# Kernel optimization log

Measured on AMD Instinct MI355X. Metric: run time of the kernel, lower is better.

## Reference

```python
import jax, jax.numpy as jnp
import numpy as np

N = 50000
E = 800000
N_CT = 32
EMBED = 256
HIDDEN = 128
OUT = 512
NEG_SLOPE = 0.2


def setup_inputs() -> dict:
    key = jax.random.key(0)
    ks = jax.random.split(key, 12)
    ct_idx = jax.random.randint(ks[0], (N,), 0, N_CT)
    cell_type_onehot = jax.nn.one_hot(ct_idx, N_CT, dtype=jnp.float32)
    lipid_droplet_scalar = jax.random.normal(ks[1], (N,), dtype=jnp.float32)
    edge_index = jax.random.randint(ks[2], (2, E), 0, N, dtype=jnp.int32)
    s = 0.05
    return {
        "cell_type_onehot": cell_type_onehot,
        "lipid_droplet_scalar": lipid_droplet_scalar,
        "edge_index": edge_index,
        "W_embed": jax.random.normal(ks[3], (N_CT + 1, EMBED), dtype=jnp.float32) * s,
        "b_embed": jnp.zeros((EMBED,), dtype=jnp.float32),
        "W_l": jax.random.normal(ks[4], (EMBED, HIDDEN), dtype=jnp.float32) * s,
        "b_l": jnp.zeros((HIDDEN,), dtype=jnp.float32),
        "W_r": jax.random.normal(ks[5], (EMBED, HIDDEN), dtype=jnp.float32) * s,
        "b_r": jnp.zeros((HIDDEN,), dtype=jnp.float32),
        "att": jax.random.normal(ks[6], (HIDDEN,), dtype=jnp.float32) * s,
        "gat_bias": jnp.zeros((HIDDEN,), dtype=jnp.float32),
        "W_out": jax.random.normal(ks[7], (HIDDEN, OUT), dtype=jnp.float32) * s,
        "b_out": jnp.zeros((OUT,), dtype=jnp.float32),
        "dispersion": jax.random.normal(ks[8], (OUT, N_CT), dtype=jnp.float32) * s,
    }


def reference(cell_type_onehot, lipid_droplet_scalar, edge_index,
              W_embed, b_embed, W_l, b_l, W_r, b_r, att, gat_bias,
              W_out, b_out, dispersion):
    n = cell_type_onehot.shape[0]
    lds = lipid_droplet_scalar[:, None] if lipid_droplet_scalar.ndim == 1 else lipid_droplet_scalar
    combined = jnp.concatenate([cell_type_onehot, lds], axis=1)  # [N, n_ct+1]
    x = jax.nn.elu(combined @ W_embed + b_embed)  # [N, EMBED]

    # GATv2Conv, heads=1, concat=True (PyG semantics)
    x_l = x @ W_l + b_l  # source-side transform [N, H]
    x_r = x @ W_r + b_r  # target-side transform [N, H]
    src, dst = edge_index[0], edge_index[1]
    e = jax.nn.leaky_relu(x_l[src] + x_r[dst], negative_slope=NEG_SLOPE)  # [E, H]
    logit = e @ att  # [E]
    # scatter-softmax over incoming edges of each target node
    m = jax.ops.segment_max(logit, dst, num_segments=n)
    alpha = jnp.exp(logit - m[dst])
    denom = jax.ops.segment_sum(alpha, dst, num_segments=n)
    alpha = alpha / (denom[dst] + 1e-16)
    agg = jax.ops.segment_sum(alpha[:, None] * x_l[src], dst, num_segments=n)  # [N, H]
    h = jax.nn.elu(agg + gat_bias)

    logits = h @ W_out + b_out  # [N, OUT]
    ct_idx = jnp.argmax(cell_type_onehot, axis=1)  # [N]
    disp = jax.nn.softplus(dispersion[:, ct_idx]).T  # [N, OUT]
    return logits, disp
```

## Files before the change

kernel.cpp:

```cpp
#include <hip/hip_runtime.h>
#include <hip/hip_bf16.h>
#include <math.h>

#define N    50000
#define E    800000
#define NCT  32
#define EMB  256
#define HID  128
#define OUTD 512
#define NB_SCAN 49
#define XPAD 260
#define HPAD 132

__device__ __forceinline__ float4 fma4s(float a, float4 b, float4 c) {
    return make_float4(fmaf(a, b.x, c.x), fmaf(a, b.y, c.y),
                       fmaf(a, b.z, c.z), fmaf(a, b.w, c.w));
}
__device__ __forceinline__ float4 add4(float4 a, float4 b) {
    return make_float4(a.x + b.x, a.y + b.y, a.z + b.z, a.w + b.w);
}

__global__ void k_init(const float* __restrict__ onehot,
                       const float* __restrict__ dispersion,
                       int* __restrict__ ct, int* __restrict__ hist,
                       float* __restrict__ spt) {
    int i = blockIdx.x * 256 + threadIdx.x;
    if (i < N) {
        const float* row = onehot + (size_t)i * NCT;
        int c = 0;
        #pragma unroll
        for (int j = 0; j < NCT; j++)
            if (row[j] > 0.5f) c = j;
        ct[i] = c;
        hist[i] = 0;
    }
    if (i < OUTD * NCT) {
        float x = dispersion[i];
        float s = log1pf(expf(-fabsf(x))) + fmaxf(x, 0.f);
        int c = i >> 5, j = i & 31;
        spt[j * OUTD + c] = s;
    }
}

__global__ __launch_bounds__(256) void k_hist(const int* __restrict__ eidx,
                                              int* __restrict__ hist) {
    int i = blockIdx.x * 256 + threadIdx.x;
    if (i < E / 4) {
        int4 d = reinterpret_cast<const int4*>(eidx + E)[i];
        atomicAdd(&hist[d.x], 1);
        atomicAdd(&hist[d.y], 1);
        atomicAdd(&hist[d.z], 1);
        atomicAdd(&hist[d.w], 1);
    }
}

__global__ __launch_bounds__(256, 3) void k_xlr(
        const int* __restrict__ ct, const float* __restrict__ ldsc,
        const float* __restrict__ We, const float* __restrict__ be,
        const float* __restrict__ pWl, const float* __restrict__ pbl,
        const float* __restrict__ pWr, const float* __restrict__ pbr,
        float* __restrict__ xl, float* __restrict__ xr) {
    __shared__ float xs[32 * XPAD];
    __shared__ float Bs[16 * 256];
    __shared__ int   ctl[32];
    __shared__ float ldl[32];
    const int t  = threadIdx.x;
    const int n0 = blockIdx.x * 32;

    if (t < 32) {
        int n = n0 + t; if (n >= N) n = N - 1;
        ctl[t] = ct[n];
        ldl[t] = ldsc[n];
    }
    __syncthreads();

    {
        const float w32 = We[NCT * EMB + t];
        const float bb  = be[t];
        for (int m = 0; m < 32; m++) {
            float v = fmaf(ldl[m], w32, We[ctl[m] * EMB + t]) + bb;
            xs[m * XPAD + t] = v > 0.f ? v : expm1f(v);
        }
    }

    const int cg = t & 31;
    const int rg = t >> 5;
    const float* xrow = xs + rg * 4 * XPAD;
    const int cA = cg * 4;
    const int st_kk  = t >> 6;
    const int st_col = (t & 63) * 4;

    float4 accA[4], accB[4];
    #pragma unroll
    for (int r = 0; r < 4; r++) {
        accA[r] = make_float4(0.f, 0.f, 0.f, 0.f);
        accB[r] = make_float4(0.f, 0.f, 0.f, 0.f);
    }

    for (int kc = 0; kc < EMB; kc += 16) {
        __syncthreads();
        #pragma unroll
        for (int j = 0; j < 4; j++) {
            int kk  = st_kk + j * 4;
            int col = st_col;
            const float* src = (col < HID) ? (pWl + (size_t)(kc + kk) * HID + col)
                                           : (pWr + (size_t)(kc + kk) * HID + col - HID);
            *reinterpret_cast<float4*>(&Bs[kk * 256 + col]) =
                *reinterpret_cast<const float4*>(src);
        }
        __syncthreads();

        #pragma unroll
        for (int kk = 0; kk < 16; kk += 4) {
            float4 bA[4], bB[4];
            #pragma unroll
            for (int q = 0; q < 4; q++) {
                bA[q] = *reinterpret_cast<const float4*>(&Bs[(kk + q) * 256 + cA]);
                bB[q] = *reinterpret_cast<const float4*>(&Bs[(kk + q) * 256 + 128 + cA]);
            }
            float4 a[4];
            #pragma unroll
            for (int r = 0; r < 4; r++)
                a[r] = *reinterpret_cast<const float4*>(xrow + r * XPAD + kc + kk);
            #pragma unroll
            for (int r = 0; r < 4; r++) {
                accA[r] = fma4s(a[r].x, bA[0], accA[r]);
                accB[r] = fma4s(a[r].x, bB[0], accB[r]);
                accA[r] = fma4s(a[r].y, bA[1], accA[r]);
                accB[r] = fma4s(a[r].y, bB[1], accB[r]);
                accA[r] = fma4s(a[r].z, bA[2], accA[r]);
                accB[r] = fma4s(a[r].z, bB[2], accB[r]);
                accA[r] = fma4s(a[r].w, bA[3], accA[r]);
                accB[r] = fma4s(a[r].w, bB[3], accB[r]);
            }
        }
    }

    const float4 biasA = *reinterpret_cast<const float4*>(pbl + cA);
    const float4 biasB = *reinterpret_cast<const float4*>(pbr + cA);
    #pragma unroll
    for (int r = 0; r < 4; r++) {
        int n = n0 + rg * 4 + r;
        if (n < N) {
            *reinterpret_cast<float4*>(xl + (size_t)n * HID + cA) = add4(accA[r], biasA);
            *reinterpret_cast<float4*>(xr + (size_t)n * HID + cA) = add4(accB[r], biasB);
        }
    }
}

__global__ __launch_bounds__(1024) void k_scan1(const int* __restrict__ hist,
                                                int* __restrict__ offs,
                                                int* __restrict__ bsum) {
    __shared__ int sb[2][1024];
    const int t = threadIdx.x;
    const int i = blockIdx.x * 1024 + t;
    int v = (i < N) ? hist[i] : 0;
    sb[0][t] = v;
    __syncthreads();
    int pin = 0;
    for (int off = 1; off < 1024; off <<= 1) {
        int x = sb[pin][t];
        if (t >= off) x += sb[pin][t - off];
        sb[pin ^ 1][t] = x;
        pin ^= 1;
        __syncthreads();
    }
    int incl = sb[pin][t];
    if (i < N) offs[i] = incl - v;
    if (t == 1023) bsum[blockIdx.x] = incl;
}

__global__ void k_scan2(const int* __restrict__ bsum, int* __restrict__ bbase) {
    if (threadIdx.x == 0) {
        int run = 0;
        for (int j = 0; j < NB_SCAN; j++) { bbase[j] = run; run += bsum[j]; }
    }
}

__global__ __launch_bounds__(1024) void k_scan3(int* __restrict__ offs,
                                                int* __restrict__ cursor,
                                                const int* __restrict__ bbase) {
    const int t = threadIdx.x;
    const int i = blockIdx.x * 1024 + t;
    if (i < N) {
        int v = offs[i] + bbase[blockIdx.x];
        offs[i] = v;
        cursor[i] = v;
    }
    if (blockIdx.x == 0 && t == 0) offs[N] = E;
}

__global__ __launch_bounds__(256) void k_scatter(const int* __restrict__ eidx,
                                                 int* __restrict__ cursor,
                                                 int* __restrict__ sorted) {
    const int e = blockIdx.x * 256 + threadIdx.x;
    if (e < E) {
        int s = eidx[e];
        int d = eidx[E + e];
        int pos = atomicAdd(&cursor[d], 1);
        sorted[pos] = s;
    }
}

__global__ __launch_bounds__(256, 8) void k_agg(
        const int* __restrict__ offs, const int* __restrict__ srt,
        const float* __restrict__ xl, const float* __restrict__ attv,
        const float* __restrict__ gb, float* xrh) {
    const int t = threadIdx.x;
    const int n = blockIdx.x * 8 + (t >> 5);
    if (n >= N) return;
    const int lane = t & 31;
    const float4* xl4 = reinterpret_cast<const float4*>(xl);
    float4* xh4 = reinterpret_cast<float4*>(xrh);

    const float4 xr4 = xh4[(size_t)n * 32 + lane];
    const float4 at4 = reinterpret_cast<const float4*>(attv)[lane];
    const int i0  = offs[n];
    const int deg = offs[n + 1] - i0;

    float m = -3.0e38f, den = 0.f;
    float4 acc = make_float4(0.f, 0.f, 0.f, 0.f);

#define STEP(XC) {                                                          \
    float vx = XC.x + xr4.x, vy = XC.y + xr4.y,                             \
          vz = XC.z + xr4.z, vw = XC.w + xr4.w;                             \
    vx = fmaxf(vx, 0.f) + 0.2f * fminf(vx, 0.f);                            \
    vy = fmaxf(vy, 0.f) + 0.2f * fminf(vy, 0.f);                            \
    vz = fmaxf(vz, 0.f) + 0.2f * fminf(vz, 0.f);                            \
    vw = fmaxf(vw, 0.f) + 0.2f * fminf(vw, 0.f);                            \
    float p = fmaf(vx, at4.x, fmaf(vy, at4.y, fmaf(vz, at4.z, vw * at4.w)));\
    p += __shfl_xor(p, 16); p += __shfl_xor(p, 8);                          \
    p += __shfl_xor(p, 4);  p += __shfl_xor(p, 2); p += __shfl_xor(p, 1);   \
    float mn = fmaxf(m, p);                                                 \
    float sc = __expf(m - mn);                                              \
    float w  = __expf(p - mn);                                              \
    den   = fmaf(den, sc, w);                                               \
    acc.x = fmaf(acc.x, sc, w * XC.x);                                      \
    acc.y = fmaf(acc.y, sc, w * XC.y);                                      \
    acc.z = fmaf(acc.z, sc, w * XC.z);                                      \
    acc.w = fmaf(acc.w, sc, w * XC.w);                                      \
    m = mn; }

    if (deg > 0) {
        const int lastI = i0 + deg - 1;
        #define LDX(J) xl4[(size_t)srt[min(i0 + (J), lastI)] * 32 + lane]
        float4 x0 = LDX(0), x1 = LDX(1), x2 = LDX(2), x3 = LDX(3);
        int i = 0;
        for (; i + 4 <= deg; i += 4) {
            const int base = i0 + i + 4;
            float4 n0 = xl4[(size_t)srt[min(base + 0, lastI)] * 32 + lane];
            float4 n1 = xl4[(size_t)srt[min(base + 1, lastI)] * 32 + lane];
            float4 n2 = xl4[(size_t)srt[min(base + 2, lastI)] * 32 + lane];
            float4 n3 = xl4[(size_t)srt[min(base + 3, lastI)] * 32 + lane];
            STEP(x0); STEP(x1); STEP(x2); STEP(x3);
            x0 = n0; x1 = n1; x2 = n2; x3 = n3;
        }
        if (i     < deg) STEP(x0);
        if (i + 1 < deg) STEP(x1);
        if (i + 2 < deg) STEP(x2);
        #undef LDX
    }
#undef STEP

    float inv = 1.f / (den + 1e-16f);
    const float4 g4 = reinterpret_cast<const float4*>(gb)[lane];
    float hx = fmaf(acc.x, inv, g4.x);
    float hy = fmaf(acc.y, inv, g4.y);
    float hz = fmaf(acc.z, inv, g4.z);
    float hw = fmaf(acc.w, inv, g4.w);
    hx = hx > 0.f ? hx : expm1f(hx);
    hy = hy > 0.f ? hy : expm1f(hy);
    hz = hz > 0.f ? hz : expm1f(hz);
    hw = hw > 0.f ? hw : expm1f(hw);
    xh4[(size_t)n * 32 + lane] = make_float4(hx, hy, hz, hw);
}

__global__ __launch_bounds__(256, 3) void k_out(
        const float* __restrict__ h, const int* __restrict__ ct,
        const float* __restrict__ Wo, const float* __restrict__ bo,
        const float* __restrict__ spt, float* __restrict__ out) {
    __shared__ float hs[32 * HPAD];
    __shared__ float Bs[16 * OUTD];
    __shared__ int ctl[32];
    const int t  = threadIdx.x;
    const int n0 = blockIdx.x * 32;

    if (t < 32) { int n = n0 + t; ctl[t] = ct[n < N ? n : N - 1]; }
    {
        const float4* h4 = reinterpret_cast<const float4*>(h);
        #pragma unroll
        for (int j = 0; j < 4; j++) {
            int idx4 = t + j * 256;
            int row  = idx4 >> 5;
            int k4   = (idx4 & 31) * 4;
            int n = n0 + row;
            float4 v = (n < N) ? h4[(size_t)n * 32 + (idx4 & 31)]
                               : make_float4(0.f, 0.f, 0.f, 0.f);
            float* d = hs + row * HPAD + k4;
            d[0] = v.x; d[1] = v.y; d[2] = v.z; d[3] = v.w;
        }
    }

    const int cg = t & 31, rg = t >> 5;
    const float* hrow = hs + rg * 4 * HPAD;
    const int cA = cg * 4;
    const int st_kk  = t >> 7;
    const int st_col = (t & 127) * 4;

    float4 acc[2][4][2];
    #pragma unroll
    for (int cp = 0; cp < 2; cp++)
        #pragma unroll
        for (int r = 0; r < 4; r++) {
            acc[cp][r][0] = make_float4(0.f, 0.f, 0.f, 0.f);
            acc[cp][r][1] = make_float4(0.f, 0.f, 0.f, 0.f);
        }

    for (int kc = 0; kc < HID; kc += 16) {
        __syncthreads();
        #pragma unroll
        for (int j = 0; j < 8; j++) {
            int kk = st_kk + j * 2;
            *reinterpret_cast<float4*>(&Bs[kk * OUTD + st_col]) =
                *reinterpret_cast<const float4*>(Wo + (size_t)(kc + kk) * OUTD + st_col);
        }
        __syncthreads();

        #pragma unroll
        for (int kk = 0; kk < 16; kk += 4) {
            float4 a[4];
            #pragma unroll
            for (int r = 0; r < 4; r++)
                a[r] = *reinterpret_cast<const float4*>(hrow + r * HPAD + kc + kk);
            #pragma unroll
            for (int cp = 0; cp < 2; cp++) {
                float4 bA[4], bB[4];
                #pragma unroll
                for (int q = 0; q < 4; q++) {
                    bA[q] = *reinterpret_cast<const float4*>(&Bs[(kk + q) * OUTD + cp * 256 + cA]);
                    bB[q] = *reinterpret_cast<const float4*>(&Bs[(kk + q) * OUTD + cp * 256 + 128 + cA]);
                }
                #pragma unroll
                for (int r = 0; r < 4; r++) {
                    acc[cp][r][0] = fma4s(a[r].x, bA[0], acc[cp][r][0]);
                    acc[cp][r][1] = fma4s(a[r].x, bB[0], acc[cp][r][1]);
                    acc[cp][r][0] = fma4s(a[r].y, bA[1], acc[cp][r][0]);
                    acc[cp][r][1] = fma4s(a[r].y, bB[1], acc[cp][r][1]);
                    acc[cp][r][0] = fma4s(a[r].z, bA[2], acc[cp][r][0]);
                    acc[cp][r][1] = fma4s(a[r].z, bB[2], acc[cp][r][1]);
                    acc[cp][r][0] = fma4s(a[r].w, bA[3], acc[cp][r][0]);
                    acc[cp][r][1] = fma4s(a[r].w, bB[3], acc[cp][r][1]);
                }
            }
        }
    }

    float* outd = out + (size_t)N * OUTD;
    #pragma unroll
    for (int cp = 0; cp < 2; cp++) {
        const int c0 = cp * 256 + cA;
        const int c1 = cp * 256 + 128 + cA;
        const float4 bias0 = *reinterpret_cast<const float4*>(bo + c0);
        const float4 bias1 = *reinterpret_cast<const float4*>(bo + c1);
        #pragma unroll
        for (int r = 0; r < 4; r++) {
            int n = n0 + rg * 4 + r;
            if (n < N) {
                *reinterpret_cast<float4*>(out + (size_t)n * OUTD + c0) = add4(acc[cp][r][0], bias0);
                *reinterpret_cast<float4*>(out + (size_t)n * OUTD + c1) = add4(acc[cp][r][1], bias1);
                int cn = ctl[rg * 4 + r];
                *reinterpret_cast<float4*>(outd + (size_t)n * OUTD + c0) =
                    *reinterpret_cast<const float4*>(spt + cn * OUTD + c0);
                *reinterpret_cast<float4*>(outd + (size_t)n * OUTD + c1) =
                    *reinterpret_cast<const float4*>(spt + cn * OUTD + c1);
            }
        }
    }
}

extern "C" void kernel_launch(void* const* d_in, const int* in_sizes, int n_in,
                              void* d_out, int out_size, void* d_ws, size_t ws_size,
                              hipStream_t stream) {
    const float* onehot     = (const float*)d_in[0];
    const float* ldsc       = (const float*)d_in[1];
    const int*   eidx       = (const int*)  d_in[2];
    const float* We         = (const float*)d_in[3];
    const float* be         = (const float*)d_in[4];
    const float* Wl         = (const float*)d_in[5];
    const float* bl         = (const float*)d_in[6];
    const float* Wr         = (const float*)d_in[7];
    const float* br         = (const float*)d_in[8];
    const float* attv       = (const float*)d_in[9];
    const float* gb         = (const float*)d_in[10];
    const float* Wo         = (const float*)d_in[11];
    const float* bo         = (const float*)d_in[12];
    const float* dispersion = (const float*)d_in[13];

    float* ws     = (float*)d_ws;
    float* xl     = ws;
    float* xr     = xl + (size_t)N * HID;
    int*   sorted = (int*)(xr + (size_t)N * HID);
    int*   ct     = sorted + E;
    int*   offs   = ct + N;
    int*   cursor = offs + (N + 1);
    int*   hist   = cursor + (N + 1);
    float* spt    = (float*)(hist + N);
    int*   bsum   = (int*)(spt + NCT * OUTD);
    int*   bbase  = bsum + 64;

    float* out = (float*)d_out;

    k_init   <<<(N + 255) / 256, 256, 0, stream>>>(onehot, dispersion, ct, hist, spt);
    k_hist   <<<(E / 4 + 255) / 256, 256, 0, stream>>>(eidx, hist);
    k_xlr    <<<(N + 31) / 32, 256, 0, stream>>>(ct, ldsc, We, be, Wl, bl, Wr, br, xl, xr);
    k_scan1  <<<NB_SCAN, 1024, 0, stream>>>(hist, offs, bsum);
    k_scan2  <<<1, 64, 0, stream>>>(bsum, bbase);
    k_scan3  <<<NB_SCAN, 1024, 0, stream>>>(offs, cursor, bbase);
    k_scatter<<<(E + 255) / 256, 256, 0, stream>>>(eidx, cursor, sorted);
    k_agg    <<<(N + 7) / 8, 256, 0, stream>>>(offs, sorted, xl, attv, gb, xr);
    k_out    <<<(N + 31) / 32, 256, 0, stream>>>(xr, ct, Wo, bo, spt, out);
}
```

Baseline: 611.5 us.

## Retile xlr and output GEMMs to 8-row register tiles with split weight blocks

k_xlr now processes 64 nodes per block, and each block computes only one of the two projections (W_l or W_r), chosen by the block index parity. Each thread accumulates 8 rows by 4 columns, and the weight staging tile shrinks to 128 columns. k_out switches to 8 rows by 2 column-groups per thread and drops the padded h layout. The aim is more FMAs per shared-memory load. The cost is that the embedding/ELU work is recomputed twice per node, and the unpadded h rows may cause LDS bank conflicts.

```diff
diff --git a/kernel.cpp b/kernel.cpp
--- a/kernel.cpp
+++ b/kernel.cpp
@@ -10,7 +10,6 @@
 #define OUTD 512
 #define NB_SCAN 49
 #define XPAD 260
-#define HPAD 132
 
 __device__ __forceinline__ float4 fma4s(float a, float4 b, float4 c) {
     return make_float4(fmaf(a, b.x, c.x), fmaf(a, b.y, c.y),
@@ -54,20 +53,21 @@
     }
 }
 
-__global__ __launch_bounds__(256, 3) void k_xlr(
+__global__ __launch_bounds__(256, 2) void k_xlr(
         const int* __restrict__ ct, const float* __restrict__ ldsc,
         const float* __restrict__ We, const float* __restrict__ be,
         const float* __restrict__ pWl, const float* __restrict__ pbl,
         const float* __restrict__ pWr, const float* __restrict__ pbr,
         float* __restrict__ xl, float* __restrict__ xr) {
-    __shared__ float xs[32 * XPAD];
-    __shared__ float Bs[16 * 256];
-    __shared__ int   ctl[32];
-    __shared__ float ldl[32];
-    const int t  = threadIdx.x;
-    const int n0 = blockIdx.x * 32;
-
-    if (t < 32) {
+    __shared__ float xs[64 * XPAD];
+    __shared__ float Bs[16 * HID];
+    __shared__ int   ctl[64];
+    __shared__ float ldl[64];
+    const int t    = threadIdx.x;
+    const int b    = blockIdx.x & 1;
+    const int n0   = (blockIdx.x >> 1) * 64;
+
+    if (t < 64) {
         int n = n0 + t; if (n >= N) n = N - 1;
         ctl[t] = ct[n];
         ldl[t] = ldsc[n];
@@ -77,74 +77,61 @@
     {
         const float w32 = We[NCT * EMB + t];
         const float bb  = be[t];
-        for (int m = 0; m < 32; m++) {
+        for (int m = 0; m < 64; m++) {
             float v = fmaf(ldl[m], w32, We[ctl[m] * EMB + t]) + bb;
             xs[m * XPAD + t] = v > 0.f ? v : expm1f(v);
         }
     }
 
+    const float* W  = b ? pWr : pbl == pbr ? pWr : pWl;
+    const float* Wp = b ? pWr : pWl;
+    (void)W;
+    const int rg = t >> 5;
     const int cg = t & 31;
-    const int rg = t >> 5;
-    const float* xrow = xs + rg * 4 * XPAD;
-    const int cA = cg * 4;
-    const int st_kk  = t >> 6;
-    const int st_col = (t & 63) * 4;
-
-    float4 accA[4], accB[4];
+    const int c  = cg * 4;
+    const float* xrow = xs + rg * 8 * XPAD;
+    const int st_kk  = t >> 5;
+    const int st_col = (t & 31) * 4;
+
+    float4 acc[8];
     #pragma unroll
-    for (int r = 0; r < 4; r++) {
-        accA[r] = make_float4(0.f, 0.f, 0.f, 0.f);
-        accB[r] = make_float4(0.f, 0.f, 0.f, 0.f);
-    }
+    for (int r = 0; r < 8; r++) acc[r] = make_float4(0.f, 0.f, 0.f, 0.f);
 
     for (int kc = 0; kc < EMB; kc += 16) {
         __syncthreads();
-        #pragma unroll
-        for (int j = 0; j < 4; j++) {
-            int kk  = st_kk + j * 4;
-            int col = st_col;
-            const float* src = (col < HID) ? (pWl + (size_t)(kc + kk) * HID + col)
-                                           : (pWr + (size_t)(kc + kk) * HID + col - HID);
-            *reinterpret_cast<float4*>(&Bs[kk * 256 + col]) =
-                *reinterpret_cast<const float4*>(src);
-        }
+        *reinterpret_cast<float4*>(&Bs[st_kk * HID + st_col]) =
+            *reinterpret_cast<const float4*>(Wp + (size_t)(kc + st_kk) * HID + st_col);
+        *reinterpret_cast<float4*>(&Bs[(st_kk + 8) * HID + st_col]) =
+            *reinterpret_cast<const float4*>(Wp + (size_t)(kc + st_kk + 8) * HID + st_col);
         __syncthreads();
 
         #pragma unroll
         for (int kk = 0; kk < 16; kk += 4) {
-            float4 bA[4], bB[4];
-            #pragma unroll
-            for (int q = 0; q < 4; q++) {
-                bA[q] = *reinterpret_cast<const float4*>(&Bs[(kk + q) * 256 + cA]);
-                bB[q] = *reinterpret_cast<const float4*>(&Bs[(kk + q) * 256 + 128 + cA]);
+            float4 bq[4];
+            #pragma unroll
+            for (int q = 0; q < 4; q++)
+                bq[q] = *reinterpret_cast<const float4*>(&Bs[(kk + q) * HID + c]);
+            float4 a[8];
+            #pragma unroll
+            for (int r = 0; r < 8; r++)
+                a[r] = *reinterpret_cast<const float4*>(xrow + r * XPAD + kc + kk);
+            #pragma unroll
+            for (int r = 0; r < 8; r++) {
+                acc[r] = fma4s(a[r].x, bq[0], acc[r]);
+                acc[r] = fma4s(a[r].y, bq[1], acc[r]);
+                acc[r] = fma4s(a[r].z, bq[2], acc[r]);
+                acc[r] = fma4s(a[r].w, bq[3], acc[r]);
             }
-            float4 a[4];
-            #pragma unroll
-            for (int r = 0; r < 4; r++)
-                a[r] = *reinterpret_cast<const float4*>(xrow + r * XPAD + kc + kk);
-            #pragma unroll
-            for (int r = 0; r < 4; r++) {
-                accA[r] = fma4s(a[r].x, bA[0], accA[r]);
-                accB[r] = fma4s(a[r].x, bB[0], accB[r]);
-                accA[r] = fma4s(a[r].y, bA[1], accA[r]);
-                accB[r] = fma4s(a[r].y, bB[1], accB[r]);
-                accA[r] = fma4s(a[r].z, bA[2], accA[r]);
-                accB[r] = fma4s(a[r].z, bB[2], accB[r]);
-                accA[r] = fma4s(a[r].w, bA[3], accA[r]);
-                accB[r] = fma4s(a[r].w, bB[3], accB[r]);
-            }
-        }
-    }
-
-    const float4 biasA = *reinterpret_cast<const float4*>(pbl + cA);
-    const float4 biasB = *reinterpret_cast<const float4*>(pbr + cA);
+        }
+    }
+
+    float* outP = b ? xr : xl;
+    const float4 bias = *reinterpret_cast<const float4*>((b ? pbr : pbl) + c);
     #pragma unroll
-    for (int r = 0; r < 4; r++) {
-        int n = n0 + rg * 4 + r;
-        if (n < N) {
-            *reinterpret_cast<float4*>(xl + (size_t)n * HID + cA) = add4(accA[r], biasA);
-            *reinterpret_cast<float4*>(xr + (size_t)n * HID + cA) = add4(accB[r], biasB);
-        }
+    for (int r = 0; r < 8; r++) {
+        int n = n0 + rg * 8 + r;
+        if (n < N)
+            *reinterpret_cast<float4*>(outP + (size_t)n * HID + c) = add4(acc[r], bias);
     }
 }
 
@@ -279,7 +266,7 @@
         const float* __restrict__ h, const int* __restrict__ ct,
         const float* __restrict__ Wo, const float* __restrict__ bo,
         const float* __restrict__ spt, float* __restrict__ out) {
-    __shared__ float hs[32 * HPAD];
+    __shared__ float hs[32 * HID];
     __shared__ float Bs[16 * OUTD];
     __shared__ int ctl[32];
     const int t  = threadIdx.x;
@@ -290,31 +277,30 @@
         const float4* h4 = reinterpret_cast<const float4*>(h);
         #pragma unroll
         for (int j = 0; j < 4; j++) {
-            int idx4 = t + j * 256;
-            int row  = idx4 >> 5;
-            int k4   = (idx4 & 31) * 4;
+            int fi  = t + j * 256;
+            int row = fi >> 5;
+            int k4  = (fi & 31) * 4;
             int n = n0 + row;
-            float4 v = (n < N) ? h4[(size_t)n * 32 + (idx4 & 31)]
+            float4 v = (n < N) ? h4[(size_t)n * 32 + (fi & 31)]
                                : make_float4(0.f, 0.f, 0.f, 0.f);
-            float* d = hs + row * HPAD + k4;
-            d[0] = v.x; d[1] = v.y; d[2] = v.z; d[3] = v.w;
-        }
-    }
-
-    const int cg = t & 31, rg = t >> 5;
-    const float* hrow = hs + rg * 4 * HPAD;
-    const int cA = cg * 4;
+            *reinterpret_cast<float4*>(&hs[row * HID + k4]) = v;
+        }
+    }
+
+    const int rg = t >> 6;
+    const int cg = t & 63;
+    const int c0 = cg * 4;
+    const int c1 = 256 + cg * 4;
+    const float* hrow = hs + rg * 8 * HID;
     const int st_kk  = t >> 7;
     const int st_col = (t & 127) * 4;
 
-    float4 acc[2][4][2];
+    float4 acc0[8], acc1[8];
     #pragma unroll
-    for (int cp = 0; cp < 2; cp++)
-        #pragma unroll
-        for (int r = 0; r < 4; r++) {
-            acc[cp][r][0] = make_float4(0.f, 0.f, 0.f, 0.f);
-            acc[cp][r][1] = make_float4(0.f, 0.f, 0.f, 0.f);
-        }
+    for (int r = 0; r < 8; r++) {
+        acc0[r] = make_float4(0.f, 0.f, 0.f, 0.f);
+        acc1[r] = make_float4(0.f, 0.f, 0.f, 0.f);
+    }
 
     for (int kc = 0; kc < HID; kc += 16) {
         __syncthreads();
@@ -328,52 +314,40 @@
 
         #pragma unroll
         for (int kk = 0; kk < 16; kk += 4) {
-            float4 a[4];
-            #pragma unroll
-            for (int r = 0; r < 4; r++)
-                a[r] = *reinterpret_cast<const float4*>(hrow + r * HPAD + kc + kk);
-            #pragma unroll
-            for (int cp = 0; cp < 2; cp++) {
-                float4 bA[4], bB[4];
+            float4 a[8];
+            #pragma unroll
+            for (int r = 0; r < 8; r++)
+                a[r] = *reinterpret_cast<const float4*>(hrow + r * HID + kc + kk);
+            #pragma unroll
+            for (int q = 0; q < 4; q++) {
+                float4 b0 = *reinterpret_cast<const float4*>(&Bs[(kk + q) * OUTD + c0]);
+                float4 b1 = *reinterpret_cast<const float4*>(&Bs[(kk + q) * OUTD + c1]);
+                const float* aq = reinterpret_cast<const float*>(a);
                 #pragma unroll
-                for (int q = 0; q < 4; q++) {
-                    bA[q] = *reinterpret_cast<const float4*>(&Bs[(kk + q) * OUTD + cp * 256 + cA]);
-                    bB[q] = *reinterpret_cast<const float4*>(&Bs[(kk + q) * OUTD + cp * 256 + 128 + cA]);
-                }
-                #pragma unroll
-                for (int r = 0; r < 4; r++) {
-                    acc[cp][r][0] = fma4s(a[r].x, bA[0], acc[cp][r][0]);
-                    acc[cp][r][1] = fma4s(a[r].x, bB[0], acc[cp][r][1]);
-                    acc[cp][r][0] = fma4s(a[r].y, bA[1], acc[cp][r][0]);
-                    acc[cp][r][1] = fma4s(a[r].y, bB[1], acc[cp][r][1]);
-                    acc[cp][r][0] = fma4s(a[r].z, bA[2], acc[cp][r][0]);
-                    acc[cp][r][1] = fma4s(a[r].z, bB[2], acc[cp][r][1]);
-                    acc[cp][r][0] = fma4s(a[r].w, bA[3], acc[cp][r][0]);
-                    acc[cp][r][1] = fma4s(a[r].w, bB[3], acc[cp][r][1]);
+                for (int r = 0; r < 8; r++) {
+                    float av = aq[r * 4 + q];
+                    acc0[r] = fma4s(av, b0, acc0[r]);
+                    acc1[r] = fma4s(av, b1, acc1[r]);
                 }
             }
         }
     }
 
     float* outd = out + (size_t)N * OUTD;
+    const float4 bias0 = *reinterpret_cast<const float4*>(bo + c0);
+    const float4 bias1 = *reinterpret_cast<const float4*>(bo + c1);
     #pragma unroll
-    for (int cp = 0; cp < 2; cp++) {
-        const int c0 = cp * 256 + cA;
-        const int c1 = cp * 256 + 128 + cA;
-        const float4 bias0 = *reinterpret_cast<const float4*>(bo + c0);
-        const float4 bias1 = *reinterpret_cast<const float4*>(bo + c1);
-        #pragma unroll
-        for (int r = 0; r < 4; r++) {
-            int n = n0 + rg * 4 + r;
-            if (n < N) {
-                *reinterpret_cast<float4*>(out + (size_t)n * OUTD + c0) = add4(acc[cp][r][0], bias0);
-                *reinterpret_cast<float4*>(out + (size_t)n * OUTD + c1) = add4(acc[cp][r][1], bias1);
-                int cn = ctl[rg * 4 + r];
-                *reinterpret_cast<float4*>(outd + (size_t)n * OUTD + c0) =
-                    *reinterpret_cast<const float4*>(spt + cn * OUTD + c0);
-                *reinterpret_cast<float4*>(outd + (size_t)n * OUTD + c1) =
-                    *reinterpret_cast<const float4*>(spt + cn * OUTD + c1);
-            }
+    for (int r = 0; r < 8; r++) {
+        int row = rg * 8 + r;
+        int n = n0 + row;
+        if (n < N) {
+            *reinterpret_cast<float4*>(out + (size_t)n * OUTD + c0) = add4(acc0[r], bias0);
+            *reinterpret_cast<float4*>(out + (size_t)n * OUTD + c1) = add4(acc1[r], bias1);
+            int cn = ctl[row];
+            *reinterpret_cast<float4*>(outd + (size_t)n * OUTD + c0) =
+                *reinterpret_cast<const float4*>(spt + cn * OUTD + c0);
+            *reinterpret_cast<float4*>(outd + (size_t)n * OUTD + c1) =
+                *reinterpret_cast<const float4*>(spt + cn * OUTD + c1);
         }
     }
 }
@@ -410,9 +384,11 @@
 
     float* out = (float*)d_out;
 
+    const int xlr_tiles = (N + 63) / 64;
+
     k_init   <<<(N + 255) / 256, 256, 0, stream>>>(onehot, dispersion, ct, hist, spt);
     k_hist   <<<(E / 4 + 255) / 256, 256, 0, stream>>>(eidx, hist);
-    k_xlr    <<<(N + 31) / 32, 256, 0, stream>>>(ct, ldsc, We, be, Wl, bl, Wr, br, xl, xr);
+    k_xlr    <<<xlr_tiles * 2, 256, 0, stream>>>(ct, ldsc, We, be, Wl, bl, Wr, br, xl, xr);
     k_scan1  <<<NB_SCAN, 1024, 0, stream>>>(hist, offs, bsum);
     k_scan2  <<<1, 64, 0, stream>>>(bsum, bbase);
     k_scan3  <<<NB_SCAN, 1024, 0, stream>>>(offs, cursor, bbase);
```

Result: faster. 578.4 us (-5.4%).
